# Performance work log

Hardware: AMD Instinct MI355X
Metric: run time of the kernel (lower is better)

Reference implementation:

```python
import jax, jax.numpy as jnp
import numpy as np

B, D, TOPC = 8, 1024, 256
CIN, DOWN, BR, NR, G = 64, 128, 2, 8, 8
GC = DOWN // G
H = W = 64
LN_EPS = 1e-5


def _ln(x, g, b):
    mu = x.mean(-1, keepdims=True)
    var = ((x - mu) ** 2).mean(-1, keepdims=True)
    return (x - mu) * jax.lax.rsqrt(var + LN_EPS) * g + b


def _gelu(x):
    return jax.nn.gelu(x, approximate=False)


def _sample_topleft(I, IX, IY, IT, x, y):
    # x, y: [B, N] continuous coords; returns [B, CIN, N]
    x = x[:, None, :]
    y = y[:, None, :]
    X = jnp.ceil(x).astype(jnp.int32)
    Y = jnp.ceil(y).astype(jnp.int32)
    z = jnp.zeros_like(X)
    dx = X - x
    dy = Y - y
    b = jnp.arange(B)[:, None, None]
    c = jnp.arange(CIN)[None, :, None]
    wx1 = 0.5 * dx ** 2
    wx2 = dx - wx1
    wy1 = 0.5 * dy ** 2
    wy2 = dy - wy1
    s_a = IT[b, c, X, Y]
    s_e1 = (wy1 * (IX[b, c, X, Y - 1] - 0.5 * I[b, c, X, Y - 1] - 0.5 * I[b, c, z, Y - 1])
            + wy2 * (IX[b, c, X, Y] - 0.5 * I[b, c, X, Y] - 0.5 * I[b, c, z, Y]))
    s_e2 = (wx1 * (IY[b, c, X - 1, Y] - 0.5 * I[b, c, X - 1, Y] - 0.5 * I[b, c, X - 1, z])
            + wx2 * (IY[b, c, X, Y] - 0.5 * I[b, c, X, Y] - 0.5 * I[b, c, X, z]))
    s_c = (wx1 * wy1 * I[b, c, X - 1, Y - 1] + wx2 * wy1 * I[b, c, X, Y - 1]
           + wx1 * wy2 * I[b, c, X - 1, Y] + wx2 * wy2 * I[b, c, X, Y])
    return s_a - s_e1 - s_e2 + s_c


def setup_inputs() -> dict:
    key = jax.random.key(0)
    ks = jax.random.split(key, 20)
    s = 0.02
    return {
        "x": jax.random.normal(ks[0], (B, D, TOPC), jnp.float32),
        "I": jax.random.normal(ks[1], (B, CIN, H, W), jnp.float32),
        "IX": jax.random.normal(ks[2], (B, CIN, H, W), jnp.float32),
        "IY": jax.random.normal(ks[3], (B, CIN, H, W), jnp.float32),
        "IT": jax.random.normal(ks[4], (B, CIN, H, W), jnp.float32),
        "w_idx": jax.random.normal(ks[5], (BR * NR * 4, TOPC), jnp.float32) * s,
        "b_idx": jnp.zeros((BR * NR * 4,), jnp.float32),
        "w_proj": jax.random.normal(ks[6], (DOWN, CIN), jnp.float32) * s,
        "b_proj": jnp.zeros((DOWN,), jnp.float32),
        "w_mask": jax.random.normal(ks[7], (BR * NR * G, TOPC), jnp.float32) * s,
        "b_mask": jnp.zeros((BR * NR * G,), jnp.float32),
        "g1": jnp.ones((DOWN,), jnp.float32),
        "beta1": jnp.zeros((DOWN,), jnp.float32),
        "w_mlp1": jax.random.normal(ks[8], (4 * DOWN, DOWN), jnp.float32) * s,
        "b_mlp1": jnp.zeros((4 * DOWN,), jnp.float32),
        "w_mlp2": jax.random.normal(ks[9], (DOWN, 4 * DOWN), jnp.float32) * s,
        "b_mlp2": jnp.zeros((DOWN,), jnp.float32),
        "g2": jnp.ones((DOWN,), jnp.float32),
        "beta2": jnp.zeros((DOWN,), jnp.float32),
    }


def reference(x, I, IX, IY, IT, w_idx, b_idx, w_proj, b_proj, w_mask, b_mask,
              g1, beta1, w_mlp1, b_mlp1, w_mlp2, b_mlp2, g2, beta2):
    # rect prediction
    p = x @ w_idx.T + b_idx                       # [B, D, BR*NR*4]
    fac = jnp.array([H - 1, W - 1, H - 1, W - 1], jnp.float32)
    p = jax.nn.sigmoid(p.reshape(B, D, BR, NR, 4)) * fac
    p = p.reshape(B, D * BR * NR, 4)
    x1, y1, x2, y2 = p[:, :, 0], p[:, :, 1], p[:, :, 2], p[:, :, 3]
    S = (_sample_topleft(I, IX, IY, IT, x2, y2)
         - _sample_topleft(I, IX, IY, IT, x1, y2)
         - _sample_topleft(I, IX, IY, IT, x2, y1)
         + _sample_topleft(I, IX, IY, IT, x1, y1))  # [B, CIN, N]
    S = S.reshape(B, CIN, D, BR, NR).transpose(0, 2, 3, 4, 1)  # [B, D, BR, NR, CIN]
    rects = _gelu(S @ w_proj.T + b_proj)           # [B, D, BR, NR, DOWN]
    mask = (x @ w_mask.T + b_mask).reshape(B, D * BR, NR, G, 1)
    mask = jax.nn.softmax(mask, axis=2)
    rects = rects.reshape(B, D * BR, NR, G, GC)
    out = (mask * rects).sum(2).reshape(B, D * BR, DOWN)
    out = _ln(out, g1, beta1)
    shortcut = out
    out = _gelu(out @ w_mlp1.T + b_mlp1) @ w_mlp2.T + b_mlp2
    return _ln(out, g2, beta2) + shortcut
```

## Files before the change

### kernel.cpp

```cpp
#include <hip/hip_runtime.h>
#include <hip/hip_bf16.h>
#include <hip/hip_fp16.h>
#include <math.h>

#define BB   8
#define DD   1024

typedef short bh8 __attribute__((ext_vector_type(8)));
typedef float f32x4 __attribute__((ext_vector_type(4)));
typedef _Float16 h2f __attribute__((ext_vector_type(2)));

__device__ __forceinline__ ushort f2bf(float f) {
    uint u = __builtin_bit_cast(uint, f);
    u += 0x7fffu + ((u >> 16) & 1u);
    return (ushort)(u >> 16);
}
__device__ __forceinline__ float asf(uint u)  { return __builtin_bit_cast(float, u); }
__device__ __forceinline__ float bflo(uint u) { return __builtin_bit_cast(float, u << 16); }
__device__ __forceinline__ float bfhi(uint u) { return __builtin_bit_cast(float, u & 0xffff0000u); }
__device__ __forceinline__ uint  pkh(float a, float b) {
    return __builtin_bit_cast(uint, __builtin_amdgcn_cvt_pkrtz(a, b));
}
__device__ __forceinline__ h2f ash2f(uint u) { return __builtin_bit_cast(h2f, u); }

#if __has_builtin(__builtin_amdgcn_fdot2)
__device__ __forceinline__ float fdot2h(h2f a, h2f b, float c) {
    return __builtin_amdgcn_fdot2(a, b, c, false);
}
#else
__device__ __forceinline__ float fdot2h(h2f a, h2f b, float c) {
    return fmaf((float)a.x, (float)b.x, fmaf((float)a.y, (float)b.y, c));
}
#endif

__device__ __forceinline__ uint cvtpk_bf16(float a, float b) {
    uint r;
    asm("v_cvt_pk_bf16_f32 %0, %1, %2" : "=v"(r) : "v"(a), "v"(b));
    return r;
}
__device__ __forceinline__ ushort cvt1_bf16(float a) {
    uint r;
    asm("v_cvt_pk_bf16_f32 %0, %1, %2" : "=v"(r) : "v"(a), "v"(a));
    return (ushort)r;
}

__device__ __forceinline__ float gelu_fast(float x) {
    float x2 = x * x;
#if __has_builtin(__builtin_amdgcn_exp2f)
    float e = __builtin_amdgcn_exp2f(x * fmaf(x2, -0.20588652f, -2.3022082f));
#else
    float e = __expf(-(1.5957691216f * x + 0.14270963f * x * x2));
#endif
    return x * __builtin_amdgcn_rcpf(1.0f + e);
}
__device__ __forceinline__ float sig63(float v) {
    return 63.0f * __builtin_amdgcn_rcpf(1.0f + __expf(-v));
}

__global__ __launch_bounds__(256) void kT_pack(
    const float* __restrict__ w_idx, const float* __restrict__ w_mask,
    const float* __restrict__ w_proj, const float* __restrict__ w1,
    const float* __restrict__ w2,
    ushort* __restrict__ catPh, ushort* __restrict__ catPm,
    ushort* __restrict__ catPl,
    ushort* __restrict__ w_projP, ushort* __restrict__ w1P,
    ushort* __restrict__ w2P)
{
    int bid = blockIdx.x, t = threadIdx.x;
    if (bid < 24) {
        int gid = bid * 256 + t;
        int l = gid & 63, ks = (gid >> 6) & 7, nt = gid >> 9;
        int n = nt * 16 + (l & 15);
        int kbase = ks * 32 + ((l >> 4) << 3);
        const float* src = (n < 64) ? (w_idx + (size_t)n * 256)
                                    : (w_mask + (size_t)(n - 64) * 256);
        ushort* dh = catPh + (size_t)gid * 8;
        ushort* dm = catPm + (size_t)gid * 8;
        ushort* dl = catPl + (size_t)gid * 8;
        #pragma unroll
        for (int j = 0; j < 8; ++j) {
            float v = src[kbase + j];
            ushort h = f2bf(v);
            float hf = __builtin_bit_cast(float, (uint)h << 16);
            float r1 = v - hf;
            ushort m = f2bf(r1); float mf = __builtin_bit_cast(float, (uint)m << 16);
            ushort lo = f2bf(r1 - mf);
            dh[j] = h; dm[j] = m; dl[j] = lo;
        }
    } else if (bid < 28) {
        int g = (bid - 24) * 256 + t;
        int nt = g >> 7, ks = (g >> 6) & 1, l = g & 63;
        int n = nt * 16 + (l & 15), k0 = ks * 32 + (l >> 4) * 8;
        ushort* dst = w_projP + (size_t)g * 8;
        #pragma unroll
        for (int j = 0; j < 8; ++j) dst[j] = f2bf(w_proj[n * 64 + k0 + j]);
    } else if (bid < 60) {
        int g = (bid - 28) * 256 + t;
        int nt = g >> 8, ks = (g >> 6) & 3, l = g & 63;
        int n = nt * 16 + (l & 15), k0 = ks * 32 + (l >> 4) * 8;
        ushort* dst = w1P + (size_t)g * 8;
        #pragma unroll
        for (int j = 0; j < 8; ++j) dst[j] = f2bf(w1[n * 128 + k0 + j]);
    } else {
        int g = (bid - 60) * 256 + t;
        int nt = g >> 10, ks = (g >> 6) & 15, l = g & 63;
        int n = nt * 16 + (l & 15), k0 = ks * 32 + (l >> 4) * 8;
        ushort* dst = w2P + (size_t)g * 8;
        #pragma unroll
        for (int j = 0; j < 8; ++j) dst[j] = f2bf(w2[n * 512 + k0 + j]);
    }
}

__global__ __launch_bounds__(256) void k01(
    const float* __restrict__ x,
    const ushort* __restrict__ catPh, const ushort* __restrict__ catPm,
    const ushort* __restrict__ catPl,
    const float* __restrict__ b_idx, const float* __restrict__ b_mask,
    float* __restrict__ maskw, uint* __restrict__ meta,
    const float* __restrict__ I, const float* __restrict__ IX,
    const float* __restrict__ IY, const float* __restrict__ IT,
    uint4* __restrict__ T1, ushort* __restrict__ T2)
{
    __shared__ __align__(16) float sf[3264];
    int t = threadIdx.x;
    int bid = blockIdx.x;

    if (bid >= 4096) {
        float* sOut = sf;
        size_t rowbase = (size_t)(bid - 4096) * 16;
        int w = t >> 6, l = t & 63;

        f32x4 acc[3];
        acc[0] = (f32x4){0.f,0.f,0.f,0.f};
        acc[1] = (f32x4){0.f,0.f,0.f,0.f};
        acc[2] = (f32x4){0.f,0.f,0.f,0.f};
        const float* xr = x + (rowbase + (size_t)(l & 15)) * 256 + ((l >> 4) << 3);

        #pragma unroll
        for (int half = 0; half < 2; ++half) {
            bh8 Ah[4], Am[4], Al[4];
            #pragma unroll
            for (int k4 = 0; k4 < 4; ++k4) {
                int ks = half * 4 + k4;
                float4 v0 = *(const float4*)(xr + ks * 32);
                float4 v1 = *(const float4*)(xr + ks * 32 + 4);
                uint4 uh, um, ul;
                uh.x = cvtpk_bf16(v0.x, v0.y);
                uh.y = cvtpk_bf16(v0.z, v0.w);
                uh.z = cvtpk_bf16(v1.x, v1.y);
                uh.w = cvtpk_bf16(v1.z, v1.w);
                float r0a = v0.x - bflo(uh.x), r0b = v0.y - bfhi(uh.x);
                float r0c = v0.z - bflo(uh.y), r0d = v0.w - bfhi(uh.y);
                float r1a = v1.x - bflo(uh.z), r1b = v1.y - bfhi(uh.z);
                float r1c = v1.z - bflo(uh.w), r1d = v1.w - bfhi(uh.w);
                um.x = cvtpk_bf16(r0a, r0b);
                um.y = cvtpk_bf16(r0c, r0d);
                um.z = cvtpk_bf16(r1a, r1b);
                um.w = cvtpk_bf16(r1c, r1d);
                ul.x = cvtpk_bf16(r0a - bflo(um.x), r0b - bfhi(um.x));
                ul.y = cvtpk_bf16(r0c - bflo(um.y), r0d - bfhi(um.y));
                ul.z = cvtpk_bf16(r1a - bflo(um.z), r1b - bfhi(um.z));
                ul.w = cvtpk_bf16(r1c - bflo(um.w), r1d - bfhi(um.w));
                Ah[k4] = __builtin_bit_cast(bh8, uh);
                Am[k4] = __builtin_bit_cast(bh8, um);
                Al[k4] = __builtin_bit_cast(bh8, ul);
            }
            #pragma unroll
            for (int ntl = 0; ntl < 3; ++ntl) {
                int nt = w * 3 + ntl;
                #pragma unroll
                for (int k4 = 0; k4 < 4; ++k4) {
                    int ks = half * 4 + k4;
                    size_t fo = ((size_t)(nt * 8 + ks) * 64 + l) * 8;
                    bh8 bh = *(const bh8*)(catPh + fo);
                    bh8 bm = *(const bh8*)(catPm + fo);
                    bh8 bl = *(const bh8*)(catPl + fo);
                    acc[ntl] = __builtin_amdgcn_mfma_f32_16x16x32_bf16(Ah[k4], bh, acc[ntl], 0, 0, 0);
                    acc[ntl] = __builtin_amdgcn_mfma_f32_16x16x32_bf16(Ah[k4], bm, acc[ntl], 0, 0, 0);
                    acc[ntl] = __builtin_amdgcn_mfma_f32_16x16x32_bf16(Am[k4], bh, acc[ntl], 0, 0, 0);
                    acc[ntl] = __builtin_amdgcn_mfma_f32_16x16x32_bf16(Ah[k4], bl, acc[ntl], 0, 0, 0);
                    acc[ntl] = __builtin_amdgcn_mfma_f32_16x16x32_bf16(Al[k4], bh, acc[ntl], 0, 0, 0);
                    acc[ntl] = __builtin_amdgcn_mfma_f32_16x16x32_bf16(Am[k4], bm, acc[ntl], 0, 0, 0);
                }
            }
        }
        {
            int r0 = (l >> 4) * 4, cbase = w * 48 + (l & 15);
            #pragma unroll
            for (int ntl = 0; ntl < 3; ++ntl)
                #pragma unroll
                for (int reg = 0; reg < 4; ++reg)
                    sOut[(r0 + reg) * 193 + cbase + ntl * 16] = acc[ntl][reg];
        }
        __syncthreads();

        {
            int row = t >> 4, u = t & 15, br = u >> 3, nr = u & 7;
            const float* so = sOut + row * 193;
            int c0 = br * 32 + nr * 4;
            float x1 = sig63(so[c0 + 0] + b_idx[c0 + 0]);
            float y1 = sig63(so[c0 + 1] + b_idx[c0 + 1]);
            float x2 = sig63(so[c0 + 2] + b_idx[c0 + 2]);
            float y2 = sig63(so[c0 + 3] + b_idx[c0 + 3]);
            int X1 = (int)ceilf(x1); X1 = X1 < 1 ? 1 : (X1 > 63 ? 63 : X1);
            int X2 = (int)ceilf(x2); X2 = X2 < 1 ? 1 : (X2 > 63 ? 63 : X2);
            int Y1 = (int)ceilf(y1); Y1 = Y1 < 1 ? 1 : (Y1 > 63 ? 63 : Y1);
            int Y2 = (int)ceilf(y2); Y2 = Y2 < 1 ? 1 : (Y2 > 63 ? 63 : Y2);
            float dxa = (float)X1 - x1, dxb = (float)X2 - x2;
            float dya = (float)Y1 - y1, dyb = (float)Y2 - y2;
            int   Xc[4] = {X2, X1, X2, X1};
            int   Yc[4] = {Y2, Y2, Y1, Y1};
            float sg[4] = {1.f, -1.f, -1.f, 1.f};
            float dxc[4] = {dxb, dxa, dxb, dxa};
            float dyc[4] = {dyb, dyb, dya, dya};
            uint* mr = meta + (((rowbase + row) * 16) + (size_t)u) * 32;
            #pragma unroll
            for (int c = 0; c < 4; ++c) {
                uint pt = (uint)(Xc[c] * 64 + Yc[c]);
                float s = sg[c], dx = dxc[c], dy = dyc[c];
                float dx2 = dx * dx, dy2 = dy * dy;
                uint4 wa, wb;
                wa.x = pt * 1024u;
                wa.y = pt * 128u;
                wa.z = pkh(s, s * dy);
                wa.w = pkh(s * dy2, s * dx);
                wb.x = pkh(s * dx2, s * dx * dy);
                wb.y = pkh(s * dx * dy2, s * dx2 * dy);
                wb.z = __builtin_bit_cast(uint, s * dx2 * dy2);
                wb.w = 0u;
                *(uint4*)(mr + c * 8 + 0) = wa;
                *(uint4*)(mr + c * 8 + 4) = wb;
            }
        }
        {
            int row = t >> 4, br = (t >> 3) & 1, g = t & 7;
            const float* so = sOut + row * 193 + 64;
            float lg[8];
            float mx = -1e30f;
            #pragma unroll
            for (int nr = 0; nr < 8; ++nr) {
                int idx = br * 64 + nr * 8 + g;
                lg[nr] = so[idx] + b_mask[idx];
                mx = fmaxf(mx, lg[nr]);
            }
            float s = 0.f;
            #pragma unroll
            for (int nr = 0; nr < 8; ++nr) { lg[nr] = __expf(lg[nr] - mx); s += lg[nr]; }
            float inv = __builtin_amdgcn_rcpf(s);
            #pragma unroll
            for (int nr = 0; nr < 8; ++nr)
                maskw[(rowbase + row) * 128 + br * 64 + nr * 8 + g] = lg[nr] * inv;
        }
    } else {
        int chunk = bid & 7, b = (bid >> 3) & 7, h = bid >> 6;
        int hp = h > 0 ? h - 1 : 0;
        int cb = chunk * 8;
        size_t inb  = (size_t)b * 262144 + (size_t)h  * 64;
        size_t inbp = (size_t)b * 262144 + (size_t)hp * 64;

        {
            int half = t >> 7;
            int pos = t & 127, c = pos >> 4, w4 = (pos & 15) << 2;
            size_t o = (size_t)(cb + c) * 4096 + w4;
            int so = c * 68 + w4;
            int base = half ? 544 : 0;
            const float* pA = half ? (I  + inbp) : (I  + inb);
            const float* pB = half ? (IY + inb)  : (IX + inb);
            const float* pC = half ? (IT + inb)  : (IY + inbp);
            *(float4*)(sf + base + so)               = *(const float4*)(pA + o);
            *(float4*)(sf + 1088 + base + so)        = *(const float4*)(pB + o);
            *(float4*)(sf + 2176 + base + so)        = *(const float4*)(pC + o);
        }
        __syncthreads();

        #pragma unroll
        for (int i = 0; i < 2; ++i) {
            int idx = i * 256 + t; int w = idx >> 3, c = idx & 7;
            int wm = w > 0 ? w - 1 : 0;
            int rb = c * 68;
            float I00 = sf[rb + w],        I0m = sf[rb + wm];
            float Im0 = sf[544 + rb + w],  Imm = sf[544 + rb + wm];
            float E1  = sf[1088 + rb + w]  - 0.5f * I00;
            float E1m = sf[1088 + rb + wm] - 0.5f * I0m;
            float E2  = sf[1632 + rb + w]  - 0.5f * I00;
            float E2m = sf[2176 + rb + w]  - 0.5f * Im0;
            float v0 = sf[2720 + rb + w];
            float v1 = -E1;
            float v2 = 0.5f * (E1 - E1m);
            float v3 = -E2;
            float v4 = 0.5f * (E2 - E2m);
            float v5 = I00;
            float v6 = 0.5f * (I0m - I00);
            float v7 = 0.5f * (Im0 - I00);
            float v8 = 0.25f * ((Imm - I0m) - (Im0 - I00));
            size_t pt = (((size_t)b * 4096) + (size_t)h * 64 + w) * 64 + (cb + c);
            uint4 o4;
            o4.x = pkh(v0, v1);
            o4.y = pkh(v2, v3);
            o4.z = pkh(v4, v5);
            o4.w = pkh(v6, v7);
            T1[pt] = o4;
            T2[pt] = (ushort)(pkh(v8, 0.f) & 0xffffu);
        }
    }
}

__global__ __launch_bounds__(256) void k2_rects(
    const uint4* __restrict__ T1, const ushort* __restrict__ T2,
    const uint* __restrict__ meta,
    const ushort* __restrict__ w_projP, const float* __restrict__ b_proj,
    const float* __restrict__ maskw, const float* __restrict__ g1,
    const float* __restrict__ beta1, float* __restrict__ mid)
{
    __shared__ __align__(16) uint meta_lds[16][32];
    __shared__ __align__(16) float S_lds[16][68];
    __shared__ float mrow[128];
    __shared__ float outr[2][128];
    int bid = blockIdx.x;
    int b = bid & 7, d = bid >> 3;
    int t = threadIdx.x, w = t >> 6, l = t & 63;
    size_t tile = (size_t)b * DD + d;
    if (t < 128) {
        uint4 mv = *(const uint4*)(meta + tile * 512 + (size_t)t * 4);
        *(uint4*)(&meta_lds[0][0] + t * 4) = mv;
    }
    if (t >= 128) mrow[t - 128] = maskw[tile * 128 + (t - 128)];

    bh8 bf[2][2];
    #pragma unroll
    for (int ni = 0; ni < 2; ++ni) {
        int nt = w * 2 + ni;
        #pragma unroll
        for (int ks = 0; ks < 2; ++ks)
            bf[ni][ks] = *(const bh8*)(w_projP + ((size_t)(nt * 2 + ks) * 64 + l) * 8);
    }
    __syncthreads();
    const char* t1b = ((const char*)T1) + ((size_t)b << 22) + (size_t)(l * 16);
    const char* t2b = ((const char*)T2) + ((size_t)b << 19) + (size_t)(l * 2);

    int m0 = w * 4;
    uint4 q[2][4]; ushort e8[2][4];
    #pragma unroll
    for (int g = 0; g < 2; ++g) {
        #pragma unroll
        for (int c = 0; c < 4; ++c) {
            uint o1 = __builtin_amdgcn_readfirstlane(meta_lds[m0 + g][c * 8 + 0]);
            uint o2 = __builtin_amdgcn_readfirstlane(meta_lds[m0 + g][c * 8 + 1]);
            q[g][c]  = *(const uint4*)(t1b + o1);
            e8[g][c] = *(const ushort*)(t2b + o2);
        }
    }
    #pragma unroll
    for (int rr = 0; rr < 4; ++rr) {
        int m = m0 + rr;
        int cur = rr & 1;
        uint4 qc[4]; ushort ec[4];
        #pragma unroll
        for (int c = 0; c < 4; ++c) { qc[c] = q[cur][c]; ec[c] = e8[cur][c]; }
        if (rr < 2) {
            int mn = m + 2;
            #pragma unroll
            for (int c = 0; c < 4; ++c) {
                uint o1 = __builtin_amdgcn_readfirstlane(meta_lds[mn][c * 8 + 0]);
                uint o2 = __builtin_amdgcn_readfirstlane(meta_lds[mn][c * 8 + 1]);
                q[cur][c]  = *(const uint4*)(t1b + o1);
                e8[cur][c] = *(const ushort*)(t2b + o2);
            }
        }
        float acc0 = 0.f, acc1 = 0.f;
        #pragma unroll
        for (int c = 0; c < 4; ++c) {
            uint cz = meta_lds[m][c * 8 + 2], cw = meta_lds[m][c * 8 + 3];
            uint bx = meta_lds[m][c * 8 + 4], by = meta_lds[m][c * 8 + 5];
            float bz = asf(meta_lds[m][c * 8 + 6]);
            float ev = __half2float(__builtin_bit_cast(__half, ec[c]));
            float cv = bz * ev;
            cv = fdot2h(ash2f(by), ash2f(qc[c].w), cv);
            cv = fdot2h(ash2f(bx), ash2f(qc[c].z), cv);
            cv = fdot2h(ash2f(cw), ash2f(qc[c].y), cv);
            cv = fdot2h(ash2f(cz), ash2f(qc[c].x), cv);
            if (c & 1) acc1 += cv; else acc0 += cv;
        }
        S_lds[m][l] = acc0 + acc1;
    }
    __syncthreads();

    int am = l & 15, q2 = l >> 4;
    bh8 a0, a1;
    {
        float4 va = *(const float4*)&S_lds[am][q2 * 8];
        float4 vb = *(const float4*)&S_lds[am][q2 * 8 + 4];
        uint4 ua;
        ua.x = cvtpk_bf16(va.x, va.y);
        ua.y = cvtpk_bf16(va.z, va.w);
        ua.z = cvtpk_bf16(vb.x, vb.y);
        ua.w = cvtpk_bf16(vb.z, vb.w);
        a0 = __builtin_bit_cast(bh8, ua);
        float4 vc = *(const float4*)&S_lds[am][32 + q2 * 8];
        float4 vd = *(const float4*)&S_lds[am][32 + q2 * 8 + 4];
        uint4 ub;
        ub.x = cvtpk_bf16(vc.x, vc.y);
        ub.y = cvtpk_bf16(vc.z, vc.w);
        ub.z = cvtpk_bf16(vd.x, vd.y);
        ub.w = cvtpk_bf16(vd.z, vd.w);
        a1 = __builtin_bit_cast(bh8, ub);
    }
    f32x4 cc[2];
    cc[0] = (f32x4){0.f, 0.f, 0.f, 0.f};
    cc[1] = (f32x4){0.f, 0.f, 0.f, 0.f};
    cc[0] = __builtin_amdgcn_mfma_f32_16x16x32_bf16(a0, bf[0][0], cc[0], 0, 0, 0);
    cc[0] = __builtin_amdgcn_mfma_f32_16x16x32_bf16(a1, bf[0][1], cc[0], 0, 0, 0);
    cc[1] = __builtin_amdgcn_mfma_f32_16x16x32_bf16(a0, bf[1][0], cc[1], 0, 0, 0);
    cc[1] = __builtin_amdgcn_mfma_f32_16x16x32_bf16(a1, bf[1][1], cc[1], 0, 0, 0);

    int cl = l & 15;
    #pragma unroll
    for (int ni = 0; ni < 2; ++ni) {
        int nt = w * 2 + ni;
        int col = nt * 16 + cl;
        float bpv = b_proj[col];
        float p = 0.f;
        #pragma unroll
        for (int reg = 0; reg < 4; ++reg) {
            int r = q2 * 4 + reg;
            float v = cc[ni][reg] + bpv;
            p += gelu_fast(v) * mrow[(r >> 3) * 64 + (r & 7) * 8 + nt];
        }
        p += __shfl_xor(p, 16, 64);
        if (q2 == 0) outr[0][col] = p;
        else if (q2 == 2) outr[1][col] = p;
    }
    __syncthreads();

    if (w < 2) {
        float v0 = outr[w][l], v1 = outr[w][l + 64];
        float s = v0 + v1, sq = v0 * v0 + v1 * v1;
        #pragma unroll
        for (int mm = 32; mm > 0; mm >>= 1) {
            s  += __shfl_xor(s, mm, 64);
            sq += __shfl_xor(sq, mm, 64);
        }
        float mu  = s * (1.0f / 128.0f);
        float var = sq * (1.0f / 128.0f) - mu * mu;
        float rs  = rsqrtf(var + 1e-5f);
        size_t ob = (tile * 2 + w) * 128;
        mid[ob + l]      = (v0 - mu) * rs * g1[l]      + beta1[l];
        mid[ob + l + 64] = (v1 - mu) * rs * g1[l + 64] + beta1[l + 64];
    }
}

__global__ __launch_bounds__(256) void k4_mlp(
    const float* __restrict__ mid, const ushort* __restrict__ w1P,
    const float* __restrict__ b1, const ushort* __restrict__ w2P,
    const float* __restrict__ b2, const float* __restrict__ g2,
    const float* __restrict__ beta2, float* __restrict__ outp)
{
    __shared__ float xr[16][132];
    __shared__ __align__(16) ushort Af[4][64][8];
    __shared__ __align__(16) ushort H[16][520];
    __shared__ float oo[16][128];
    __shared__ float b1s[512];
    __shared__ float b2s[128], g2s[128], bt2s[128];
    int t = threadIdx.x, w = t >> 6, l = t & 63;
    int bid = blockIdx.x;
    int mt = (bid & 7) * 128 + (bid >> 3);
    size_t rowbase = (size_t)mt * 16;

    {
        const float4* mg = (const float4*)(mid + rowbase * 128);
        #pragma unroll
        for (int i4 = 0; i4 < 2; ++i4) {
            int i = i4 * 256 + t;
            float4 v = mg[i];
            *(float4*)(&xr[i >> 5][(i & 31) * 4]) = v;
        }
    }
    for (int i = t; i < 512; i += 256) b1s[i] = b1[i];
    if (t < 128) { b2s[t] = b2[t]; g2s[t] = g2[t]; bt2s[t] = beta2[t]; }
    __syncthreads();

    {
        int ks = t >> 6, m = l & 15, c0 = ks * 32 + (l >> 4) * 8;
        uint* dst = (uint*)&Af[ks][l][0];
        #pragma unroll
        for (int j = 0; j < 4; ++j)
            dst[j] = cvtpk_bf16(xr[m][c0 + 2 * j], xr[m][c0 + 2 * j + 1]);
    }
    __syncthreads();

    f32x4 c1[8];
    #pragma unroll
    for (int i = 0; i < 8; ++i) c1[i] = (f32x4){0.f, 0.f, 0.f, 0.f};
    bh8 a[4];
    #pragma unroll
    for (int ks = 0; ks < 4; ++ks) a[ks] = *(const bh8*)&Af[ks][l][0];
    #pragma unroll
    for (int ni = 0; ni < 8; ++ni) {
        int nt = w * 8 + ni;
        #pragma unroll
        for (int ks = 0; ks < 4; ++ks) {
            bh8 bfr = *(const bh8*)(w1P + ((size_t)(nt * 4 + ks) * 64 + l) * 8);
            c1[ni] = __builtin_amdgcn_mfma_f32_16x16x32_bf16(a[ks], bfr, c1[ni], 0, 0, 0);
        }
    }
    #pragma unroll
    for (int ni = 0; ni < 8; ++ni) {
        int nt = w * 8 + ni;
        int col = nt * 16 + (l & 15);
        int r0 = (l >> 4) * 4;
        #pragma unroll
        for (int reg = 0; reg < 4; ++reg)
            H[r0 + reg][col] = cvt1_bf16(gelu_fast(c1[ni][reg] + b1s[col]));
    }
    __syncthreads();

    f32x4 c2[2];
    c2[0] = (f32x4){0.f, 0.f, 0.f, 0.f};
    c2[1] = (f32x4){0.f, 0.f, 0.f, 0.f};
    const char* hb = (const char*)&H[0][0];
    #pragma unroll
    for (int ks2 = 0; ks2 < 16; ++ks2) {
        bh8 af = *(const bh8*)(hb + (l & 15) * 1040 + ks2 * 64 + (l >> 4) * 16);
        #pragma unroll
        for (int i = 0; i < 2; ++i) {
            int nt2 = w * 2 + i;
            bh8 bfr = *(const bh8*)(w2P + ((size_t)(nt2 * 16 + ks2) * 64 + l) * 8);
            c2[i] = __builtin_amdgcn_mfma_f32_16x16x32_bf16(af, bfr, c2[i], 0, 0, 0);
        }
    }
    #pragma unroll
    for (int i = 0; i < 2; ++i) {
        int col = (w * 2 + i) * 16 + (l & 15);
        int r0 = (l >> 4) * 4;
        #pragma unroll
        for (int reg = 0; reg < 4; ++reg) oo[r0 + reg][col] = c2[i][reg] + b2s[col];
    }
    __syncthreads();

    #pragma unroll
    for (int rr = 0; rr < 4; ++rr) {
        int r = w * 4 + rr;
        float v0 = oo[r][l], v1 = oo[r][l + 64];
        float s = v0 + v1, sq = v0 * v0 + v1 * v1;
        #pragma unroll
        for (int m = 32; m > 0; m >>= 1) {
            s  += __shfl_xor(s, m, 64);
            sq += __shfl_xor(sq, m, 64);
        }
        float mu  = s * (1.0f / 128.0f);
        float var = sq * (1.0f / 128.0f) - mu * mu;
        float rs  = rsqrtf(var + 1e-5f);
        size_t ob = (rowbase + r) * 128;
        outp[ob + l]      = (v0 - mu) * rs * g2s[l]      + bt2s[l]      + xr[r][l];
        outp[ob + l + 64] = (v1 - mu) * rs * g2s[l + 64] + bt2s[l + 64] + xr[r][l + 64];
    }
}

extern "C" void kernel_launch(void* const* d_in, const int* in_sizes, int n_in,
                              void* d_out, int out_size, void* d_ws, size_t ws_size,
                              hipStream_t stream) {
    const float* x      = (const float*)d_in[0];
    const float* I      = (const float*)d_in[1];
    const float* IX     = (const float*)d_in[2];
    const float* IY     = (const float*)d_in[3];
    const float* IT     = (const float*)d_in[4];
    const float* w_idx  = (const float*)d_in[5];
    const float* b_idx  = (const float*)d_in[6];
    const float* w_proj = (const float*)d_in[7];
    const float* b_proj = (const float*)d_in[8];
    const float* w_mask = (const float*)d_in[9];
    const float* b_mask = (const float*)d_in[10];
    const float* g1     = (const float*)d_in[11];
    const float* beta1  = (const float*)d_in[12];
    const float* w_mlp1 = (const float*)d_in[13];
    const float* b_mlp1 = (const float*)d_in[14];
    const float* w_mlp2 = (const float*)d_in[15];
    const float* b_mlp2 = (const float*)d_in[16];
    const float* g2     = (const float*)d_in[17];
    const float* beta2  = (const float*)d_in[18];
    float* out = (float*)d_out;

    float* ws = (float*)d_ws;
    ushort* catPh  = (ushort*)ws;
    ushort* catPm  = (ushort*)(ws + 24576);
    ushort* catPl  = (ushort*)(ws + 49152);
    ushort* w_projP = (ushort*)(ws + 73728);
    ushort* w1P     = (ushort*)(ws + 77824);
    ushort* w2P     = (ushort*)(ws + 110592);
    float*  maskw   = ws + 143360;
    uint*   meta    = (uint*)(ws + 1191936);
    uint4*  T1      = (uint4*)(ws + 5386240);
    ushort* T2      = (ushort*)(ws + 13774848);

    kT_pack<<<92, 256, 0, stream>>>(w_idx, w_mask, w_proj, w_mlp1, w_mlp2,
                                    catPh, catPm, catPl, w_projP, w1P, w2P);
    k01<<<4608, 256, 0, stream>>>(x, catPh, catPm, catPl, b_idx, b_mask,
                                  maskw, meta, I, IX, IY, IT, T1, T2);
    k2_rects<<<8192, 256, 0, stream>>>(T1, T2, meta, w_projP, b_proj, maskw,
                                       g1, beta1, out);
    k4_mlp<<<1024, 256, 0, stream>>>(out, w1P, b_mlp1, w2P, b_mlp2, g2, beta2, out);
}
```

Baseline: 94.97 us.

## Compute integral-table prep from registers with shuffles instead of LDS staging

```diff
diff --git a/kernel.cpp b/kernel.cpp
--- a/kernel.cpp
+++ b/kernel.cpp
@@ -125,9 +125,9 @@
     int t = threadIdx.x;
     int bid = blockIdx.x;
 
-    if (bid >= 4096) {
+    if (bid >= 2048) {
         float* sOut = sf;
-        size_t rowbase = (size_t)(bid - 4096) * 16;
+        size_t rowbase = (size_t)(bid - 2048) * 16;
         int w = t >> 6, l = t & 63;
 
         f32x4 acc[3];
@@ -252,39 +252,46 @@
                 maskw[(rowbase + row) * 128 + br * 64 + nr * 8 + g] = lg[nr] * inv;
         }
     } else {
-        int chunk = bid & 7, b = (bid >> 3) & 7, h = bid >> 6;
+        int cg = bid & 3, h = (bid >> 2) & 63, b = bid >> 8;
         int hp = h > 0 ? h - 1 : 0;
-        int cb = chunk * 8;
-        size_t inb  = (size_t)b * 262144 + (size_t)h  * 64;
-        size_t inbp = (size_t)b * 262144 + (size_t)hp * 64;
-
-        {
-            int half = t >> 7;
-            int pos = t & 127, c = pos >> 4, w4 = (pos & 15) << 2;
-            size_t o = (size_t)(cb + c) * 4096 + w4;
-            int so = c * 68 + w4;
-            int base = half ? 544 : 0;
-            const float* pA = half ? (I  + inbp) : (I  + inb);
-            const float* pB = half ? (IY + inb)  : (IX + inb);
-            const float* pC = half ? (IT + inb)  : (IY + inbp);
-            *(float4*)(sf + base + so)               = *(const float4*)(pA + o);
-            *(float4*)(sf + 1088 + base + so)        = *(const float4*)(pB + o);
-            *(float4*)(sf + 2176 + base + so)        = *(const float4*)(pC + o);
-        }
-        __syncthreads();
-
-        #pragma unroll
-        for (int i = 0; i < 2; ++i) {
-            int idx = i * 256 + t; int w = idx >> 3, c = idx & 7;
-            int wm = w > 0 ? w - 1 : 0;
-            int rb = c * 68;
-            float I00 = sf[rb + w],        I0m = sf[rb + wm];
-            float Im0 = sf[544 + rb + w],  Imm = sf[544 + rb + wm];
-            float E1  = sf[1088 + rb + w]  - 0.5f * I00;
-            float E1m = sf[1088 + rb + wm] - 0.5f * I0m;
-            float E2  = sf[1632 + rb + w]  - 0.5f * I00;
-            float E2m = sf[2176 + rb + w]  - 0.5f * Im0;
-            float v0 = sf[2720 + rb + w];
+        int c = cg * 16 + (t >> 4);
+        int lane16 = t & 15;
+        int w0 = lane16 * 4;
+        size_t rowb  = (size_t)b * 262144 + (size_t)c * 4096 + (size_t)h  * 64 + w0;
+        size_t rowbp = (size_t)b * 262144 + (size_t)c * 4096 + (size_t)hp * 64 + w0;
+
+        float4 Ih  = *(const float4*)(I  + rowb);
+        float4 Ihp = *(const float4*)(I  + rowbp);
+        float4 Xh  = *(const float4*)(IX + rowb);
+        float4 Yh  = *(const float4*)(IY + rowb);
+        float4 Yhp = *(const float4*)(IY + rowbp);
+        float4 Th  = *(const float4*)(IT + rowb);
+
+        float pI  = __shfl_up(Ih.w,  1, 16);
+        float pIp = __shfl_up(Ihp.w, 1, 16);
+        float pX  = __shfl_up(Xh.w,  1, 16);
+        if (lane16 == 0) { pI = Ih.x; pIp = Ihp.x; pX = Xh.x; }
+
+        float Iv[4]  = {Ih.x, Ih.y, Ih.z, Ih.w};
+        float Ipv[4] = {Ihp.x, Ihp.y, Ihp.z, Ihp.w};
+        float Xv[4]  = {Xh.x, Xh.y, Xh.z, Xh.w};
+        float Yv[4]  = {Yh.x, Yh.y, Yh.z, Yh.w};
+        float Ypv[4] = {Yhp.x, Yhp.y, Yhp.z, Yhp.w};
+        float Tv[4]  = {Th.x, Th.y, Th.z, Th.w};
+
+        size_t ptb = (((size_t)b * 4096) + (size_t)h * 64 + w0) * 64 + c;
+        #pragma unroll
+        for (int j = 0; j < 4; ++j) {
+            float I00 = Iv[j];
+            float I0m = (j == 0) ? pI  : Iv[j - 1];
+            float Im0 = Ipv[j];
+            float Imm = (j == 0) ? pIp : Ipv[j - 1];
+            float Xm  = (j == 0) ? pX  : Xv[j - 1];
+            float E1  = Xv[j] - 0.5f * I00;
+            float E1m = Xm    - 0.5f * I0m;
+            float E2  = Yv[j]  - 0.5f * I00;
+            float E2m = Ypv[j] - 0.5f * Im0;
+            float v0 = Tv[j];
             float v1 = -E1;
             float v2 = 0.5f * (E1 - E1m);
             float v3 = -E2;
@@ -293,14 +300,13 @@
             float v6 = 0.5f * (I0m - I00);
             float v7 = 0.5f * (Im0 - I00);
             float v8 = 0.25f * ((Imm - I0m) - (Im0 - I00));
-            size_t pt = (((size_t)b * 4096) + (size_t)h * 64 + w) * 64 + (cb + c);
             uint4 o4;
             o4.x = pkh(v0, v1);
             o4.y = pkh(v2, v3);
             o4.z = pkh(v4, v5);
             o4.w = pkh(v6, v7);
-            T1[pt] = o4;
-            T2[pt] = (ushort)(pkh(v8, 0.f) & 0xffffu);
+            T1[ptb + (size_t)j * 64] = o4;
+            T2[ptb + (size_t)j * 64] = (ushort)(pkh(v8, 0.f) & 0xffffu);
         }
     }
 }
@@ -594,7 +600,7 @@
 
     kT_pack<<<92, 256, 0, stream>>>(w_idx, w_mask, w_proj, w_mlp1, w_mlp2,
                                     catPh, catPm, catPl, w_projP, w1P, w2P);
-    k01<<<4608, 256, 0, stream>>>(x, catPh, catPm, catPl, b_idx, b_mask,
+    k01<<<2560, 256, 0, stream>>>(x, catPh, catPm, catPl, b_idx, b_mask,
                                   maskw, meta, I, IX, IY, IT, T1, T2);
     k2_rects<<<8192, 256, 0, stream>>>(T1, T2, meta, w_projP, b_proj, maskw,
                                        g1, beta1, out);
```

New measurement: 93.82 us. Within noise of the previous version (-1.2%).
